# Kernel optimization log

Measured on AMD Instinct MI355X. Metric: run time of the kernel, lower is better.

Reference implementation:

```python
import jax, jax.numpy as jnp
import numpy as np

N_NODES = 50000
N_EDGES = 800000
IN_CH = 128
OUT_CH = 64  # hidden = 2*OUT_CH = 128


def setup_inputs() -> dict:
    key = jax.random.key(0)
    ks = jax.random.split(key, 5)
    x = jax.random.normal(ks[0], (N_NODES, IN_CH), dtype=jnp.float32)
    edge_index = jax.random.randint(ks[1], (2, N_EDGES), 0, N_NODES, dtype=jnp.int32)
    # Glorot-ish scaled weights for the two GCNConv layers
    W1 = jax.random.normal(ks[2], (IN_CH, 2 * OUT_CH), dtype=jnp.float32) * 0.05
    b1 = jnp.zeros((2 * OUT_CH,), dtype=jnp.float32)
    W2 = jax.random.normal(ks[3], (2 * OUT_CH, OUT_CH), dtype=jnp.float32) * 0.05
    b2 = jnp.zeros((OUT_CH,), dtype=jnp.float32)
    return {"x": x, "edge_index": edge_index, "W1": W1, "b1": b1, "W2": W2, "b2": b2}


def reference(x, edge_index, W1, b1, W2, b2):
    N = x.shape[0]
    # GCN normalization with self-loops (PyG GCNConv default):
    # A_hat = A + I, deg from target nodes, norm = d_i^-1/2 * d_j^-1/2
    loops = jnp.arange(N, dtype=edge_index.dtype)
    row = jnp.concatenate([edge_index[0], loops])  # source
    col = jnp.concatenate([edge_index[1], loops])  # target
    deg = jax.ops.segment_sum(jnp.ones(row.shape, x.dtype), col, num_segments=N)
    dinv = jnp.where(deg > 0, jax.lax.rsqrt(deg), 0.0)
    norm = dinv[row] * dinv[col]  # [E+N]

    def conv(h, W, b):
        h = h @ W                           # [N, D_out] transform first (D_out <= D_in path)
        msg = norm[:, None] * h[row]        # gather + scale: [E+N, D_out]
        agg = jax.ops.segment_sum(msg, col, num_segments=N)
        return agg + b

    h = jax.nn.relu(conv(x, W1, b1))
    return conv(h, W2, b2)
```

## Files before the change

kernel.cpp:

```cpp
#include <hip/hip_runtime.h>
#include <hip/hip_bf16.h>
#include <hip/hip_fp16.h>

#define IN_CH  128
#define HID    128
#define OUTC   64

#define NSCAT 256
#define SLOTC 64
#define CAPB  6144
#define CAP2  6144
#define TSTRIDE 140

typedef _Float16 half8 __attribute__((ext_vector_type(8)));
typedef _Float16 half4v __attribute__((ext_vector_type(4)));
typedef float float4v __attribute__((ext_vector_type(4)));

__device__ __forceinline__ void vacc(float4v& a0, float4v& a1, half8 u) {
    half4v lo = __builtin_shufflevector(u, u, 0, 1, 2, 3);
    half4v hi = __builtin_shufflevector(u, u, 4, 5, 6, 7);
    a0 += __builtin_convertvector(lo, float4v);
    a1 += __builtin_convertvector(hi, float4v);
}
__device__ __forceinline__ void vaccw(float4v& a0, float4v& a1, half8 u, float w) {
    half4v lo = __builtin_shufflevector(u, u, 0, 1, 2, 3);
    half4v hi = __builtin_shufflevector(u, u, 4, 5, 6, 7);
    a0 += w * __builtin_convertvector(lo, float4v);
    a1 += w * __builtin_convertvector(hi, float4v);
}

__global__ __launch_bounds__(256) void scatA_kernel(
        const int* __restrict__ src, const int* __restrict__ dst,
        unsigned* __restrict__ tmp2, ushort* __restrict__ cnts,
        const float* __restrict__ W1, const float* __restrict__ W2,
        _Float16* __restrict__ Wt1, _Float16* __restrict__ Wt2,
        int E, int N, int NBK, int chunk) {
    __shared__ int cnt[256];
    int t = threadIdx.x, blk = blockIdx.x;
    cnt[t] = 0;
    __syncthreads();
    int base = blk * chunk;
    int end = base + chunk; if (end > E) end = E;
    for (int e = base + t; e < end; e += 256) {
        unsigned d = (unsigned)dst[e];
        unsigned s = (unsigned)src[e];
        int b = d >> 8;
        int pos = atomicAdd(&cnt[b], 1);
        if (pos < SLOTC)
            tmp2[((size_t)(b << 8) + blk) * SLOTC + pos] = (d << 16) | s;
    }
    __syncthreads();
    if (t < NBK) {
        int c = cnt[t]; if (c > SLOTC) c = SLOTC;
        cnts[t * 256 + blk] = (ushort)c;
    }

    for (int idx = blk * 256 + t; idx < 128 * 128 + 128 * 64; idx += NSCAT * 256) {
        if (idx < 128 * 128) {
            int k = idx >> 7, nn = idx & 127;
            Wt1[nn * 128 + k] = (_Float16)W1[idx];
        } else {
            int j = idx - 128 * 128;
            int k = j >> 6, nn = j & 63;
            Wt2[nn * 128 + k] = (_Float16)W2[j];
        }
    }
}

__global__ __launch_bounds__(256) void csrB_kernel(
        const unsigned* __restrict__ tmp2, const ushort* __restrict__ cnts,
        int* __restrict__ off, ushort* __restrict__ degs, float* __restrict__ dinv,
        ushort* __restrict__ srcs,
        const float* __restrict__ x, _Float16* __restrict__ xh,
        int N, int NBK) {
    __shared__ int ex[257];
    __shared__ int h[256], cur[256];
    __shared__ unsigned ein[CAP2];
    __shared__ ushort outb[CAP2];
    __shared__ float dsh[256];
    int b = blockIdx.x, t = threadIdx.x;

    int c = cnts[b * 256 + t];
    h[t] = c;
    __syncthreads();
    for (int d = 1; d < 256; d <<= 1) {
        int v = (t >= d) ? h[t - d] : 0;
        __syncthreads();
        h[t] += v;
        __syncthreads();
    }
    ex[t] = h[t] - c;
    if (t == 255) ex[256] = h[255];
    __syncthreads();
    int total = ex[256]; if (total > CAP2) total = CAP2;

    for (int i = t; i < total; i += 256) {
        int lo = 0, hi = 255;
        while (lo < hi) {
            int mid = (lo + hi + 1) >> 1;
            if (ex[mid] <= i) lo = mid; else hi = mid - 1;
        }
        ein[i] = tmp2[((size_t)(b << 8) + lo) * SLOTC + (i - ex[lo])];
    }
    __syncthreads();

    h[t] = 0;
    __syncthreads();
    for (int i = t; i < total; i += 256)
        atomicAdd(&h[(ein[i] >> 16) & 255], 1);
    __syncthreads();
    int cdeg = h[t];
    for (int d = 1; d < 256; d <<= 1) {
        int v = (t >= d) ? h[t - d] : 0;
        __syncthreads();
        h[t] += v;
        __syncthreads();
    }
    int excl = h[t] - cdeg;
    int node = (b << 8) + t;
    float dv = rsqrtf((float)(cdeg + 1));
    if (node < N) {
        off[node] = b * CAPB + excl;
        degs[node] = (ushort)cdeg;
        dinv[node] = dv;
    }
    dsh[t] = (node < N) ? dv : 0.f;
    cur[t] = excl;
    __syncthreads();
    for (int i = t; i < total; i += 256) {
        unsigned v = ein[i];
        int pos = atomicAdd(&cur[(v >> 16) & 255], 1);
        outb[pos] = (ushort)(v & 0xFFFFu);
    }
    __syncthreads();
    for (int i = t; i < total; i += 256) srcs[b * CAPB + i] = outb[i];

    int rowbase = b << 8;
    for (int m = t; m < 256 * 16; m += 256) {
        int r = m >> 4, k = m & 15;
        int nd = rowbase + r;
        if (nd < N) {
            const float4* xp = (const float4*)(x + (size_t)nd * 128 + k * 8);
            float4 v0 = xp[0], v1 = xp[1];
            float di = dsh[r];
            half8 o = { (_Float16)(di * v0.x), (_Float16)(di * v0.y),
                        (_Float16)(di * v0.z), (_Float16)(di * v0.w),
                        (_Float16)(di * v1.x), (_Float16)(di * v1.y),
                        (_Float16)(di * v1.z), (_Float16)(di * v1.w) };
            ((half8*)xh)[(size_t)nd * 16 + k] = o;
        }
    }
}

__global__ __launch_bounds__(256) void agg1gemm_kernel(
        const _Float16* __restrict__ xh,
        const int* __restrict__ off, const ushort* __restrict__ degs,
        const ushort* __restrict__ srcs, const float* __restrict__ dinv,
        const _Float16* __restrict__ Wt1, const float* __restrict__ b1,
        const _Float16* __restrict__ Wt2, _Float16* __restrict__ H3s, int N) {
    __shared__ _Float16 tile[4][32 * TSTRIDE];
    int t = threadIdx.x;
    int grp = t >> 4, p = t & 15;
    int base = blockIdx.x * 128;
    const half8* xs = (const half8*)xh;

    for (int it = 0; it < 8; ++it) {
        int r = grp * 8 + it;
        int node = base + r;
        if (node < N) {
            int s = off[node];
            int e = s + degs[node];
            float4v a0 = (float4v)0.f, a1 = (float4v)0.f;
            float4v c0 = (float4v)0.f, c1 = (float4v)0.f;
            int j = s;
            for (; j + 8 <= e; j += 8) {
                int i0 = srcs[j], i1 = srcs[j+1], i2 = srcs[j+2], i3 = srcs[j+3];
                int i4 = srcs[j+4], i5 = srcs[j+5], i6 = srcs[j+6], i7 = srcs[j+7];
                half8 u0 = xs[(size_t)i0 * 16 + p];
                half8 u1 = xs[(size_t)i1 * 16 + p];
                half8 u2 = xs[(size_t)i2 * 16 + p];
                half8 u3 = xs[(size_t)i3 * 16 + p];
                half8 u4 = xs[(size_t)i4 * 16 + p];
                half8 u5 = xs[(size_t)i5 * 16 + p];
                half8 u6 = xs[(size_t)i6 * 16 + p];
                half8 u7 = xs[(size_t)i7 * 16 + p];
                vacc(a0, a1, u0); vacc(c0, c1, u1);
                vacc(a0, a1, u2); vacc(c0, c1, u3);
                vacc(a0, a1, u4); vacc(c0, c1, u5);
                vacc(a0, a1, u6); vacc(c0, c1, u7);
            }
            if (j + 4 <= e) {
                int i0 = srcs[j], i1 = srcs[j+1], i2 = srcs[j+2], i3 = srcs[j+3];
                half8 u0 = xs[(size_t)i0 * 16 + p];
                half8 u1 = xs[(size_t)i1 * 16 + p];
                half8 u2 = xs[(size_t)i2 * 16 + p];
                half8 u3 = xs[(size_t)i3 * 16 + p];
                vacc(a0, a1, u0); vacc(c0, c1, u1);
                vacc(a0, a1, u2); vacc(c0, c1, u3);
                j += 4;
            }
            int rm = e - j;
            if (rm > 0) {
                int i0 = srcs[j];
                int i1 = srcs[rm > 1 ? j + 1 : j];
                int i2 = srcs[rm > 2 ? j + 2 : j];
                float w1 = (rm > 1) ? 1.f : 0.f;
                float w2 = (rm > 2) ? 1.f : 0.f;
                half8 u0 = xs[(size_t)i0 * 16 + p];
                half8 u1 = xs[(size_t)i1 * 16 + p];
                half8 u2 = xs[(size_t)i2 * 16 + p];
                vacc(a0, a1, u0);
                vaccw(c0, c1, u1, w1);
                vaccw(c0, c1, u2, w2);
            }
            a0 += c0; a1 += c1;
            half8 sv = xs[(size_t)node * 16 + p];
            half4v slo = __builtin_shufflevector(sv, sv, 0, 1, 2, 3);
            half4v shi = __builtin_shufflevector(sv, sv, 4, 5, 6, 7);
            a0 += __builtin_convertvector(slo, float4v);
            a1 += __builtin_convertvector(shi, float4v);
            float di = dinv[node];
            a0 *= di; a1 *= di;
            half4v h0 = __builtin_convertvector(a0, half4v);
            half4v h1 = __builtin_convertvector(a1, half4v);
            _Float16* twp = &tile[r >> 5][(r & 31) * TSTRIDE + p * 8];
            *(half4v*)twp = h0;
            *(half4v*)(twp + 4) = h1;
        }
    }
    __syncthreads();

    int wave = t >> 6;
    int lane = t & 63;
    int n16 = lane & 15;
    int q   = lane >> 4;
    int rowBase = base + wave * 32;
    _Float16* tw = &tile[wave][0];

    half8 a[2][4];
#pragma unroll
    for (int rt = 0; rt < 2; ++rt) {
        const _Float16* ap = tw + (rt * 16 + n16) * TSTRIDE + q * 8;
#pragma unroll
        for (int kb = 0; kb < 4; ++kb)
            a[rt][kb] = *(const half8*)(ap + kb * 32);
    }

    float4v acc1[2][8];
#pragma unroll
    for (int rt = 0; rt < 2; ++rt)
#pragma unroll
        for (int ct = 0; ct < 8; ++ct) acc1[rt][ct] = (float4v)0.f;
#pragma unroll
    for (int ct = 0; ct < 8; ++ct) {
        const _Float16* bp = Wt1 + (size_t)(ct * 16 + n16) * 128 + q * 8;
        half8 b[4];
#pragma unroll
        for (int kb = 0; kb < 4; ++kb) b[kb] = *(const half8*)(bp + kb * 32);
#pragma unroll
        for (int kb = 0; kb < 4; ++kb) {
            acc1[0][ct] = __builtin_amdgcn_mfma_f32_16x16x32_f16(a[0][kb], b[kb], acc1[0][ct], 0, 0, 0);
            acc1[1][ct] = __builtin_amdgcn_mfma_f32_16x16x32_f16(a[1][kb], b[kb], acc1[1][ct], 0, 0, 0);
        }
    }

#pragma unroll
    for (int ct = 0; ct < 8; ++ct) {
        int col = ct * 16 + n16;
        float bv = b1[col];
#pragma unroll
        for (int rt = 0; rt < 2; ++rt)
#pragma unroll
            for (int r = 0; r < 4; ++r) {
                int row = rt * 16 + q * 4 + r;
                tw[row * TSTRIDE + col] = (_Float16)fmaxf(acc1[rt][ct][r] + bv, 0.f);
            }
    }
    __syncthreads();

    half8 a2[2][4];
#pragma unroll
    for (int rt = 0; rt < 2; ++rt) {
        const _Float16* tp = tw + (rt * 16 + n16) * TSTRIDE + q * 8;
#pragma unroll
        for (int kb = 0; kb < 4; ++kb)
            a2[rt][kb] = *(const half8*)(tp + kb * 32);
    }

    float4v acc2[2][4];
#pragma unroll
    for (int rt = 0; rt < 2; ++rt)
#pragma unroll
        for (int ct = 0; ct < 4; ++ct) acc2[rt][ct] = (float4v)0.f;
#pragma unroll
    for (int ct = 0; ct < 4; ++ct) {
        const _Float16* bp = Wt2 + (size_t)(ct * 16 + n16) * 128 + q * 8;
        half8 b[4];
#pragma unroll
        for (int kb = 0; kb < 4; ++kb) b[kb] = *(const half8*)(bp + kb * 32);
#pragma unroll
        for (int kb = 0; kb < 4; ++kb) {
            acc2[0][ct] = __builtin_amdgcn_mfma_f32_16x16x32_f16(a2[0][kb], b[kb], acc2[0][ct], 0, 0, 0);
            acc2[1][ct] = __builtin_amdgcn_mfma_f32_16x16x32_f16(a2[1][kb], b[kb], acc2[1][ct], 0, 0, 0);
        }
    }

#pragma unroll
    for (int rt = 0; rt < 2; ++rt)
#pragma unroll
        for (int ct = 0; ct < 4; ++ct) {
            int col = ct * 16 + n16;
#pragma unroll
            for (int r = 0; r < 4; ++r) {
                int row = rowBase + rt * 16 + q * 4 + r;
                if (row < N)
                    H3s[(size_t)row * OUTC + col] = (_Float16)(acc2[rt][ct][r] * dinv[row]);
            }
        }
}

__global__ __launch_bounds__(256) void agg2_kernel(const _Float16* __restrict__ H3s,
                                                   const int* __restrict__ off,
                                                   const ushort* __restrict__ degs,
                                                   const ushort* __restrict__ srcs,
                                                   const float* __restrict__ dinv,
                                                   const float* __restrict__ bias,
                                                   float* __restrict__ out, int N) {
    int grp = threadIdx.x >> 3;
    int p   = threadIdx.x & 7;
    int node = blockIdx.x * 32 + grp;
    if (node >= N) return;
    int s = off[node];
    int e = s + degs[node];

    const half8* hs = (const half8*)H3s;
    float4v a0 = (float4v)0.f, a1 = (float4v)0.f;
    float4v c0 = (float4v)0.f, c1 = (float4v)0.f;

    int j = s;
    for (; j + 8 <= e; j += 8) {
        int i0 = srcs[j], i1 = srcs[j+1], i2 = srcs[j+2], i3 = srcs[j+3];
        int i4 = srcs[j+4], i5 = srcs[j+5], i6 = srcs[j+6], i7 = srcs[j+7];
        half8 u0 = hs[(size_t)i0 * 8 + p];
        half8 u1 = hs[(size_t)i1 * 8 + p];
        half8 u2 = hs[(size_t)i2 * 8 + p];
        half8 u3 = hs[(size_t)i3 * 8 + p];
        half8 u4 = hs[(size_t)i4 * 8 + p];
        half8 u5 = hs[(size_t)i5 * 8 + p];
        half8 u6 = hs[(size_t)i6 * 8 + p];
        half8 u7 = hs[(size_t)i7 * 8 + p];
        vacc(a0, a1, u0); vacc(c0, c1, u1);
        vacc(a0, a1, u2); vacc(c0, c1, u3);
        vacc(a0, a1, u4); vacc(c0, c1, u5);
        vacc(a0, a1, u6); vacc(c0, c1, u7);
    }
    if (j + 4 <= e) {
        int i0 = srcs[j], i1 = srcs[j+1], i2 = srcs[j+2], i3 = srcs[j+3];
        half8 u0 = hs[(size_t)i0 * 8 + p];
        half8 u1 = hs[(size_t)i1 * 8 + p];
        half8 u2 = hs[(size_t)i2 * 8 + p];
        half8 u3 = hs[(size_t)i3 * 8 + p];
        vacc(a0, a1, u0); vacc(c0, c1, u1);
        vacc(a0, a1, u2); vacc(c0, c1, u3);
        j += 4;
    }
    int rm = e - j;
    if (rm > 0) {
        int i0 = srcs[j];
        int i1 = srcs[rm > 1 ? j + 1 : j];
        int i2 = srcs[rm > 2 ? j + 2 : j];
        float w1 = (rm > 1) ? 1.f : 0.f;
        float w2 = (rm > 2) ? 1.f : 0.f;
        half8 u0 = hs[(size_t)i0 * 8 + p];
        half8 u1 = hs[(size_t)i1 * 8 + p];
        half8 u2 = hs[(size_t)i2 * 8 + p];
        vacc(a0, a1, u0);
        vaccw(c0, c1, u1, w1);
        vaccw(c0, c1, u2, w2);
    }
    a0 += c0; a1 += c1;

    float di = dinv[node];
    half8 sv = hs[(size_t)node * 8 + p];
    half4v slo = __builtin_shufflevector(sv, sv, 0, 1, 2, 3);
    half4v shi = __builtin_shufflevector(sv, sv, 4, 5, 6, 7);
    a0 += __builtin_convertvector(slo, float4v);
    a1 += __builtin_convertvector(shi, float4v);
    const float4v* bp = (const float4v*)(bias + p * 8);
    float4v o0 = di * a0 + bp[0];
    float4v o1 = di * a1 + bp[1];
    float4v* op = (float4v*)(out + (size_t)node * 64 + p * 8);
    op[0] = o0; op[1] = o1;
}

extern "C" void kernel_launch(void* const* d_in, const int* in_sizes, int n_in,
                              void* d_out, int out_size, void* d_ws, size_t ws_size,
                              hipStream_t stream) {
    const float* x   = (const float*)d_in[0];
    const int*   ei  = (const int*)d_in[1];
    const float* W1  = (const float*)d_in[2];
    const float* b1  = (const float*)d_in[3];
    const float* W2  = (const float*)d_in[4];
    const float* b2  = (const float*)d_in[5];
    float* out = (float*)d_out;

    const int N = in_sizes[0] / IN_CH;
    const int E = in_sizes[1] / 2;
    const int* src = ei;
    const int* dst = ei + E;

    const int NBK = (N + 255) >> 8;
    const int chunk = (E + NSCAT - 1) / NSCAT;

    auto align256 = [](size_t v) { return (v + 255) & ~(size_t)255; };
    char* w = (char*)d_ws;
    int* off = (int*)w;              w += align256((size_t)N * 4);
    ushort* degs = (ushort*)w;       w += align256((size_t)N * 2);
    float* dinv = (float*)w;         w += align256((size_t)N * 4);
    ushort* cnts = (ushort*)w;       w += align256((size_t)NBK * 256 * 2);
    ushort* srcs = (ushort*)w;       w += align256((size_t)NBK * CAPB * 2);
    _Float16* Wt1 = (_Float16*)w;    w += align256((size_t)HID * 128 * 2);
    _Float16* Wt2 = (_Float16*)w;    w += align256((size_t)OUTC * 128 * 2);
    size_t reg1 = align256((size_t)NBK * 256 * SLOTC * 4);
    unsigned* tmp2 = (unsigned*)w;
    _Float16* H3s = (_Float16*)w;    w += reg1;
    _Float16* xh = (_Float16*)w;     w += align256((size_t)N * HID * 2);

    scatA_kernel<<<NSCAT, 256, 0, stream>>>(src, dst, tmp2, cnts,
                                            W1, W2, Wt1, Wt2, E, N, NBK, chunk);
    csrB_kernel<<<NBK, 256, 0, stream>>>(tmp2, cnts, off, degs, dinv, srcs,
                                         x, xh, N, NBK);

    agg1gemm_kernel<<<(N + 127) / 128, 256, 0, stream>>>(xh, off, degs, srcs, dinv,
                                                         Wt1, b1, Wt2, H3s, N);
    agg2_kernel<<<(N + 31) / 32, 256, 0, stream>>>(H3s, off, degs, srcs, dinv, b2, out, N);
}
```

Measured before the change: 189.1 us.

## Split fused layer-1 aggregation+GEMM into separate gather and MFMA GEMM kernels

Result: faster. 181.3 us (-4.1%).

```diff
diff --git a/kernel.cpp b/kernel.cpp
--- a/kernel.cpp
+++ b/kernel.cpp
@@ -152,95 +152,96 @@
     }
 }
 
-__global__ __launch_bounds__(256) void agg1gemm_kernel(
-        const _Float16* __restrict__ xh,
-        const int* __restrict__ off, const ushort* __restrict__ degs,
-        const ushort* __restrict__ srcs, const float* __restrict__ dinv,
-        const _Float16* __restrict__ Wt1, const float* __restrict__ b1,
-        const _Float16* __restrict__ Wt2, _Float16* __restrict__ H3s, int N) {
+__global__ __launch_bounds__(256, 8) void agg1_kernel(const _Float16* __restrict__ xh,
+                                                      const int* __restrict__ off,
+                                                      const ushort* __restrict__ degs,
+                                                      const ushort* __restrict__ srcs,
+                                                      const float* __restrict__ dinv,
+                                                      _Float16* __restrict__ A1, int N) {
+    int grp = threadIdx.x >> 4;
+    int p   = threadIdx.x & 15;
+    int node = blockIdx.x * 16 + grp;
+    if (node >= N) return;
+    int s = off[node];
+    int e = s + degs[node];
+
+    const half8* xs = (const half8*)xh;
+    float4v a0 = (float4v)0.f, a1 = (float4v)0.f;
+    float4v c0 = (float4v)0.f, c1 = (float4v)0.f;
+
+    int j = s;
+    for (; j + 8 <= e; j += 8) {
+        int i0 = srcs[j], i1 = srcs[j+1], i2 = srcs[j+2], i3 = srcs[j+3];
+        int i4 = srcs[j+4], i5 = srcs[j+5], i6 = srcs[j+6], i7 = srcs[j+7];
+        half8 u0 = xs[(size_t)i0 * 16 + p];
+        half8 u1 = xs[(size_t)i1 * 16 + p];
+        half8 u2 = xs[(size_t)i2 * 16 + p];
+        half8 u3 = xs[(size_t)i3 * 16 + p];
+        half8 u4 = xs[(size_t)i4 * 16 + p];
+        half8 u5 = xs[(size_t)i5 * 16 + p];
+        half8 u6 = xs[(size_t)i6 * 16 + p];
+        half8 u7 = xs[(size_t)i7 * 16 + p];
+        vacc(a0, a1, u0); vacc(c0, c1, u1);
+        vacc(a0, a1, u2); vacc(c0, c1, u3);
+        vacc(a0, a1, u4); vacc(c0, c1, u5);
+        vacc(a0, a1, u6); vacc(c0, c1, u7);
+    }
+    if (j + 4 <= e) {
+        int i0 = srcs[j], i1 = srcs[j+1], i2 = srcs[j+2], i3 = srcs[j+3];
+        half8 u0 = xs[(size_t)i0 * 16 + p];
+        half8 u1 = xs[(size_t)i1 * 16 + p];
+        half8 u2 = xs[(size_t)i2 * 16 + p];
+        half8 u3 = xs[(size_t)i3 * 16 + p];
+        vacc(a0, a1, u0); vacc(c0, c1, u1);
+        vacc(a0, a1, u2); vacc(c0, c1, u3);
+        j += 4;
+    }
+    int rm = e - j;
+    if (rm > 0) {
+        int i0 = srcs[j];
+        int i1 = srcs[rm > 1 ? j + 1 : j];
+        int i2 = srcs[rm > 2 ? j + 2 : j];
+        float w1 = (rm > 1) ? 1.f : 0.f;
+        float w2 = (rm > 2) ? 1.f : 0.f;
+        half8 u0 = xs[(size_t)i0 * 16 + p];
+        half8 u1 = xs[(size_t)i1 * 16 + p];
+        half8 u2 = xs[(size_t)i2 * 16 + p];
+        vacc(a0, a1, u0);
+        vaccw(c0, c1, u1, w1);
+        vaccw(c0, c1, u2, w2);
+    }
+    a0 += c0; a1 += c1;
+
+    float di = dinv[node];
+    half8 sv = xs[(size_t)node * 16 + p];
+    half4v slo = __builtin_shufflevector(sv, sv, 0, 1, 2, 3);
+    half4v shi = __builtin_shufflevector(sv, sv, 4, 5, 6, 7);
+    a0 += __builtin_convertvector(slo, float4v);
+    a1 += __builtin_convertvector(shi, float4v);
+    a0 *= di; a1 *= di;
+    half4v h0 = __builtin_convertvector(a0, half4v);
+    half4v h1 = __builtin_convertvector(a1, half4v);
+    half8 hh = __builtin_shufflevector(h0, h1, 0, 1, 2, 3, 4, 5, 6, 7);
+    *((half8*)(A1 + (size_t)node * 128) + p) = hh;
+}
+
+__global__ __launch_bounds__(256) void gemm_fused_kernel(
+        const _Float16* __restrict__ A1, const _Float16* __restrict__ Wt1,
+        const float* __restrict__ b1, const _Float16* __restrict__ Wt2,
+        const float* __restrict__ dinv, _Float16* __restrict__ H3s, int N) {
     __shared__ _Float16 tile[4][32 * TSTRIDE];
-    int t = threadIdx.x;
-    int grp = t >> 4, p = t & 15;
-    int base = blockIdx.x * 128;
-    const half8* xs = (const half8*)xh;
-
-    for (int it = 0; it < 8; ++it) {
-        int r = grp * 8 + it;
-        int node = base + r;
-        if (node < N) {
-            int s = off[node];
-            int e = s + degs[node];
-            float4v a0 = (float4v)0.f, a1 = (float4v)0.f;
-            float4v c0 = (float4v)0.f, c1 = (float4v)0.f;
-            int j = s;
-            for (; j + 8 <= e; j += 8) {
-                int i0 = srcs[j], i1 = srcs[j+1], i2 = srcs[j+2], i3 = srcs[j+3];
-                int i4 = srcs[j+4], i5 = srcs[j+5], i6 = srcs[j+6], i7 = srcs[j+7];
-                half8 u0 = xs[(size_t)i0 * 16 + p];
-                half8 u1 = xs[(size_t)i1 * 16 + p];
-                half8 u2 = xs[(size_t)i2 * 16 + p];
-                half8 u3 = xs[(size_t)i3 * 16 + p];
-                half8 u4 = xs[(size_t)i4 * 16 + p];
-                half8 u5 = xs[(size_t)i5 * 16 + p];
-                half8 u6 = xs[(size_t)i6 * 16 + p];
-                half8 u7 = xs[(size_t)i7 * 16 + p];
-                vacc(a0, a1, u0); vacc(c0, c1, u1);
-                vacc(a0, a1, u2); vacc(c0, c1, u3);
-                vacc(a0, a1, u4); vacc(c0, c1, u5);
-                vacc(a0, a1, u6); vacc(c0, c1, u7);
-            }
-            if (j + 4 <= e) {
-                int i0 = srcs[j], i1 = srcs[j+1], i2 = srcs[j+2], i3 = srcs[j+3];
-                half8 u0 = xs[(size_t)i0 * 16 + p];
-                half8 u1 = xs[(size_t)i1 * 16 + p];
-                half8 u2 = xs[(size_t)i2 * 16 + p];
-                half8 u3 = xs[(size_t)i3 * 16 + p];
-                vacc(a0, a1, u0); vacc(c0, c1, u1);
-                vacc(a0, a1, u2); vacc(c0, c1, u3);
-                j += 4;
-            }
-            int rm = e - j;
-            if (rm > 0) {
-                int i0 = srcs[j];
-                int i1 = srcs[rm > 1 ? j + 1 : j];
-                int i2 = srcs[rm > 2 ? j + 2 : j];
-                float w1 = (rm > 1) ? 1.f : 0.f;
-                float w2 = (rm > 2) ? 1.f : 0.f;
-                half8 u0 = xs[(size_t)i0 * 16 + p];
-                half8 u1 = xs[(size_t)i1 * 16 + p];
-                half8 u2 = xs[(size_t)i2 * 16 + p];
-                vacc(a0, a1, u0);
-                vaccw(c0, c1, u1, w1);
-                vaccw(c0, c1, u2, w2);
-            }
-            a0 += c0; a1 += c1;
-            half8 sv = xs[(size_t)node * 16 + p];
-            half4v slo = __builtin_shufflevector(sv, sv, 0, 1, 2, 3);
-            half4v shi = __builtin_shufflevector(sv, sv, 4, 5, 6, 7);
-            a0 += __builtin_convertvector(slo, float4v);
-            a1 += __builtin_convertvector(shi, float4v);
-            float di = dinv[node];
-            a0 *= di; a1 *= di;
-            half4v h0 = __builtin_convertvector(a0, half4v);
-            half4v h1 = __builtin_convertvector(a1, half4v);
-            _Float16* twp = &tile[r >> 5][(r & 31) * TSTRIDE + p * 8];
-            *(half4v*)twp = h0;
-            *(half4v*)(twp + 4) = h1;
-        }
-    }
-    __syncthreads();
-
-    int wave = t >> 6;
-    int lane = t & 63;
+    int wave = threadIdx.x >> 6;
+    int lane = threadIdx.x & 63;
     int n16 = lane & 15;
     int q   = lane >> 4;
-    int rowBase = base + wave * 32;
-    _Float16* tw = &tile[wave][0];
+    int rowBase = blockIdx.x * 128 + wave * 32;
 
     half8 a[2][4];
 #pragma unroll
     for (int rt = 0; rt < 2; ++rt) {
-        const _Float16* ap = tw + (rt * 16 + n16) * TSTRIDE + q * 8;
+        int row = rowBase + rt * 16 + n16;
+        if (row >= N) row = N - 1;
+        const _Float16* ap = A1 + (size_t)row * 128 + q * 8;
 #pragma unroll
         for (int kb = 0; kb < 4; ++kb)
             a[rt][kb] = *(const half8*)(ap + kb * 32);
@@ -264,6 +265,7 @@
         }
     }
 
+    _Float16* tw = &tile[wave][0];
 #pragma unroll
     for (int ct = 0; ct < 8; ++ct) {
         int col = ct * 16 + n16;
@@ -319,13 +321,13 @@
         }
 }
 
-__global__ __launch_bounds__(256) void agg2_kernel(const _Float16* __restrict__ H3s,
-                                                   const int* __restrict__ off,
-                                                   const ushort* __restrict__ degs,
-                                                   const ushort* __restrict__ srcs,
-                                                   const float* __restrict__ dinv,
-                                                   const float* __restrict__ bias,
-                                                   float* __restrict__ out, int N) {
+__global__ __launch_bounds__(256, 8) void agg2_kernel(const _Float16* __restrict__ H3s,
+                                                      const int* __restrict__ off,
+                                                      const ushort* __restrict__ degs,
+                                                      const ushort* __restrict__ srcs,
+                                                      const float* __restrict__ dinv,
+                                                      const float* __restrict__ bias,
+                                                      float* __restrict__ out, int N) {
     int grp = threadIdx.x >> 3;
     int p   = threadIdx.x & 7;
     int node = blockIdx.x * 32 + grp;
@@ -422,16 +424,18 @@
     _Float16* Wt1 = (_Float16*)w;    w += align256((size_t)HID * 128 * 2);
     _Float16* Wt2 = (_Float16*)w;    w += align256((size_t)OUTC * 128 * 2);
     size_t reg1 = align256((size_t)NBK * 256 * SLOTC * 4);
+    if (reg1 < align256((size_t)N * HID * 2)) reg1 = align256((size_t)N * HID * 2);
     unsigned* tmp2 = (unsigned*)w;
-    _Float16* H3s = (_Float16*)w;    w += reg1;
-    _Float16* xh = (_Float16*)w;     w += align256((size_t)N * HID * 2);
+    _Float16* A1 = (_Float16*)w;     w += reg1;
+    _Float16* xh = (_Float16*)w;
+    _Float16* H3s = (_Float16*)w;    w += align256((size_t)N * HID * 2);
 
     scatA_kernel<<<NSCAT, 256, 0, stream>>>(src, dst, tmp2, cnts,
                                             W1, W2, Wt1, Wt2, E, N, NBK, chunk);
     csrB_kernel<<<NBK, 256, 0, stream>>>(tmp2, cnts, off, degs, dinv, srcs,
                                          x, xh, N, NBK);
 
-    agg1gemm_kernel<<<(N + 127) / 128, 256, 0, stream>>>(xh, off, degs, srcs, dinv,
-                                                         Wt1, b1, Wt2, H3s, N);
+    agg1_kernel<<<(N + 15) / 16, 256, 0, stream>>>(xh, off, degs, srcs, dinv, A1, N);
+    gemm_fused_kernel<<<(N + 127) / 128, 256, 0, stream>>>(A1, Wt1, b1, Wt2, dinv, H3s, N);
     agg2_kernel<<<(N + 31) / 32, 256, 0, stream>>>(H3s, off, degs, srcs, dinv, b2, out, N);
 }
```
